# Performance work log

Measured on AMD Instinct MI355X. Metric: run time of the kernel, lower is better.

## Reference

```python
import jax, jax.numpy as jnp
import numpy as np

N = 50000      # nodes
E = 800000     # edges
C = 32         # channels (in = hidden = out, hardcoded in module)
KS = 4         # spline kernel size per dim
K = KS ** 3    # total spline kernel weights (dim=3)
H = 8          # NodeFormer heads
DH = C // H    # head dim = 4
M = 32         # random features for softmax kernel
EPS = 1e-5
SLOPE = 0.01   # LeakyReLU default
TAU = 1.0      # forward default


def seg_sum(vals, segs, num):
    return jax.ops.segment_sum(vals, segs, num_segments=num)


def leaky(x):
    return jnp.where(x >= 0, x, SLOPE * x)


def batch_norm(x, gamma, beta):
    # BatchNorm1d in training mode over the node dim (biased variance)
    mu = x.mean(0)
    var = x.var(0)
    return (x - mu) * jax.lax.rsqrt(var + EPS) * gamma + beta


def spline_conv(x, edge_index, pseudo, w_kernel, w_root, bias):
    # Degree-1 open B-spline conv (torch_spline_conv semantics), mean aggregation.
    src, dst = edge_index[0], edge_index[1]
    x_src = x[src]                                  # [E, C] gather
    p = pseudo * (KS - 1)                           # [E, 3], pseudo in [0,1]
    f = jnp.clip(jnp.floor(p), 0, KS - 2).astype(jnp.int32)
    frac = p - f                                    # [E, 3]
    buf = jnp.zeros((N * K, C), x.dtype)            # [N*K, C] per-kernel scatter buffer
    for bits in range(8):                           # 2^dim nonzero basis products
        idx = jnp.zeros(E, jnp.int32)
        basis = jnp.ones(E, x.dtype)
        for d in range(3):
            bit = (bits >> d) & 1
            idx = idx + (f[:, d] + bit) * (KS ** d)
            basis = basis * (frac[:, d] if bit else (1.0 - frac[:, d]))
        buf = buf + seg_sum(basis[:, None] * x_src, dst.astype(jnp.int32) * K + idx, N * K)
    buf = buf.reshape(N, K, C)
    deg = jnp.clip(seg_sum(jnp.ones(E, x.dtype), dst, N), 1.0)
    out = jnp.einsum('nkc,kcd->nd', buf, w_kernel) / deg[:, None]
    return out + x @ w_root + bias


def softmax_kernel(x, wp):
    # Positive random-feature map approximating the softmax kernel. x: [N,H,DH]
    xn = x / (DH ** 0.25)
    proj = jnp.einsum('nhd,hdm->nhm', xn, wp)
    sq = 0.5 * jnp.sum(xn * xn, -1, keepdims=True)
    return jnp.exp(proj - sq) / np.float32(np.sqrt(M))


def nodeformer_conv(x, edge_index, wqkv, wp, b_rel, wo, bo, gumbel, tau):
    # Kernelized Gumbel-softmax linear attention over all nodes + edge relational bias.
    q = jnp.einsum('nc,chd->nhd', x, wqkv[0])
    k = jnp.einsum('nc,chd->nhd', x, wqkv[1])
    v = jnp.einsum('nc,chd->nhd', x, wqkv[2])
    phi_q = softmax_kernel(q, wp)                              # [N,H,M]
    phi_k = softmax_kernel(k, wp) * jnp.exp(gumbel / tau)      # gumbel: [N,H,1]
    kv = jnp.einsum('nhm,nhd->hmd', phi_k, v)                  # [H,M,DH] summary
    num = jnp.einsum('nhm,hmd->nhd', phi_q, kv)
    den = jnp.einsum('nhm,hm->nh', phi_q, phi_k.sum(0)) + 1e-6
    attn = num / den[..., None]                                # [N,H,DH]
    # relational bias along observed edges (deg-normalized message passing)
    src, dst = edge_index[0], edge_index[1]
    deg = jnp.clip(seg_sum(jnp.ones(E, x.dtype), dst, N), 1.0)
    norm_e = jax.lax.rsqrt(deg[src] * deg[dst])
    rel = seg_sum(v[src] * norm_e[:, None, None], dst, N)      # [N,H,DH]
    out = attn + jax.nn.sigmoid(b_rel)[None, :, None] * rel
    return out.reshape(N, H * DH) @ wo + bo


def setup_inputs() -> dict:
    key = jax.random.key(0)
    ks = jax.random.split(key, 24)
    s_k = np.float32(1.0 / np.sqrt(C))
    inp = {
        'patch_embs': jax.random.normal(ks[0], (N, C), jnp.float32),
        'edge_index': jax.random.randint(ks[1], (2, E), 0, N),
        'edge_attr': jax.random.uniform(ks[2], (E, 3), jnp.float32),
        # SplineConv 1 & 2 params
        'w_sp1': jax.random.normal(ks[3], (K, C, C), jnp.float32) * s_k,
        'root1': jax.random.normal(ks[4], (C, C), jnp.float32) * s_k,
        'bias1': jnp.zeros((C,), jnp.float32),
        'w_sp2': jax.random.normal(ks[5], (K, C, C), jnp.float32) * s_k,
        'root2': jax.random.normal(ks[6], (C, C), jnp.float32) * s_k,
        'bias2': jnp.zeros((C,), jnp.float32),
        # 4 BatchNorm layers, packed
        'bn_gamma': jnp.ones((4, C), jnp.float32),
        'bn_beta': jnp.zeros((4, C), jnp.float32),
        # NodeFormer layer 1
        'nf1_wqkv': jax.random.normal(ks[7], (3, C, H, DH), jnp.float32) * s_k,
        'nf1_wp': jax.random.normal(ks[8], (H, DH, M), jnp.float32),
        'nf1_brel': jnp.zeros((H,), jnp.float32),
        'nf1_wo': jax.random.normal(ks[9], (H * DH, C), jnp.float32) * s_k,
        'nf1_bo': jnp.zeros((C,), jnp.float32),
        'gumbel1': -jnp.log(-jnp.log(jax.random.uniform(ks[10], (N, H, 1), jnp.float32) + 1e-9) + 1e-9),
        # NodeFormer layer 2
        'nf2_wqkv': jax.random.normal(ks[11], (3, C, H, DH), jnp.float32) * s_k,
        'nf2_wp': jax.random.normal(ks[12], (H, DH, M), jnp.float32),
        'nf2_brel': jnp.zeros((H,), jnp.float32),
        'nf2_wo': jax.random.normal(ks[13], (H * DH, C), jnp.float32) * s_k,
        'nf2_bo': jnp.zeros((C,), jnp.float32),
        'gumbel2': -jnp.log(-jnp.log(jax.random.uniform(ks[14], (N, H, 1), jnp.float32) + 1e-9) + 1e-9),
    }
    return inp


def reference(patch_embs, edge_index, edge_attr,
              w_sp1, root1, bias1, w_sp2, root2, bias2,
              bn_gamma, bn_beta,
              nf1_wqkv, nf1_wp, nf1_brel, nf1_wo, nf1_bo, gumbel1,
              nf2_wqkv, nf2_wp, nf2_brel, nf2_wo, nf2_bo, gumbel2):
    x = batch_norm(leaky(spline_conv(patch_embs, edge_index, edge_attr, w_sp1, root1, bias1)), bn_gamma[0], bn_beta[0])
    x = batch_norm(leaky(spline_conv(x, edge_index, edge_attr, w_sp2, root2, bias2)), bn_gamma[1], bn_beta[1])
    x = batch_norm(leaky(nodeformer_conv(x, edge_index, nf1_wqkv, nf1_wp, nf1_brel, nf1_wo, nf1_bo, gumbel1, TAU)), bn_gamma[2], bn_beta[2])
    x = batch_norm(nodeformer_conv(x, edge_index, nf2_wqkv, nf2_wp, nf2_brel, nf2_wo, nf2_bo, gumbel2, TAU), bn_gamma[3], bn_beta[3])
    return x
```

## Files before the change

### kernel.cpp

```cpp
#include <hip/hip_runtime.h>
#include <hip/hip_bf16.h>
#include <hip/hip_fp16.h>

#define NN 50000
#define NE 800000

__device__ __forceinline__ void gAdd(float* p, float v) {
    unsafeAtomicAdd(p, v);
}
__device__ __forceinline__ unsigned short f2bf(float f) {
    unsigned u = __float_as_uint(f);
    u += 0x7FFF + ((u >> 16) & 1);
    return (unsigned short)(u >> 16);
}

__global__ void k_hist(const int* __restrict__ ei, int* __restrict__ cnt) {
    int e = blockIdx.x * 256 + threadIdx.x;
    atomicAdd(&cnt[ei[NE + e]], 1);
}

__global__ void __launch_bounds__(1024) k_scan(const int* __restrict__ cnt,
                                               int* __restrict__ rowptr,
                                               int* __restrict__ fill,
                                               float* __restrict__ degf) {
    __shared__ int wsum[16];
    int tid = threadIdx.x;
    int wave = tid >> 6, lane = tid & 63;
    int carry = 0;
    for (int base = 0; base < NN; base += 8192) {
        int i0 = base + tid * 8;
        int v[8], pre[8], s = 0;
#pragma unroll
        for (int j = 0; j < 8; j++) {
            int i = i0 + j;
            v[j] = (i < NN) ? cnt[i] : 0;
            pre[j] = s; s += v[j];
        }
        int sc = s;
#pragma unroll
        for (int d = 1; d < 64; d <<= 1) {
            int t = __shfl_up(sc, d);
            if (lane >= d) sc += t;
        }
        if (lane == 63) wsum[wave] = sc;
        __syncthreads();
        int wpre = 0, total = 0;
#pragma unroll
        for (int w = 0; w < 16; w++) {
            int x = wsum[w];
            if (w < wave) wpre += x;
            total += x;
        }
        int excl = carry + wpre + (sc - s);
#pragma unroll
        for (int j = 0; j < 8; j++) {
            int i = i0 + j;
            if (i < NN) {
                int st = excl + pre[j];
                rowptr[i] = st;
                fill[i]   = st;
                degf[i]   = (float)(v[j] > 0 ? v[j] : 1);
                if (i == NN - 1) rowptr[NN] = st + v[j];
            }
        }
        carry += total;
        __syncthreads();
    }
}

__global__ void k_scatter(const int* __restrict__ ei, const float* __restrict__ attr,
                          const float* __restrict__ degf,
                          int* __restrict__ fill, int* __restrict__ sedgeP,
                          float2* __restrict__ re2) {
    int e = blockIdx.x * 256 + threadIdx.x;
    int src = ei[e], dst = ei[NE + e];
    int pos = atomicAdd(&fill[dst], 1);
    float p0 = attr[e * 3 + 0] * 3.f, p1 = attr[e * 3 + 1] * 3.f, p2 = attr[e * 3 + 2] * 3.f;
    float f0 = fmaxf(fminf(floorf(p0), 2.f), 0.f);
    float f1 = fmaxf(fminf(floorf(p1), 2.f), 0.f);
    float f2 = fmaxf(fminf(floorf(p2), 2.f), 0.f);
    float r0 = p0 - f0, r1 = p1 - f1, r2 = p2 - f2;
    int idxb = (int)f0 + 4 * (int)f1 + 16 * (int)f2;
    unsigned hw[8];
#pragma unroll
    for (int bits = 0; bits < 8; bits++) {
        int b0 = bits & 1, b1 = (bits >> 1) & 1, b2 = (bits >> 2) & 1;
        float bas = (b0 ? r0 : 1.f - r0) * (b1 ? r1 : 1.f - r1) * (b2 ? r2 : 1.f - r2);
        hw[bits] = (unsigned)__half_as_ushort(__float2half(bas));
    }
    int b = pos * 8;
    sedgeP[b + 0] = src;
    sedgeP[b + 1] = idxb;
    sedgeP[b + 2] = (int)(hw[0] | (hw[1] << 16));
    sedgeP[b + 3] = (int)(hw[2] | (hw[3] << 16));
    sedgeP[b + 4] = (int)(hw[4] | (hw[5] << 16));
    sedgeP[b + 5] = (int)(hw[6] | (hw[7] << 16));
    re2[pos] = make_float2(__int_as_float(src), rsqrtf(degf[src] * degf[dst]));
}

__global__ void k_cvt(const float* __restrict__ xin, unsigned short* __restrict__ xh) {
    int i = blockIdx.x * 256 + threadIdx.x;
    xh[i] = f2bf(xin[i]);
}

__global__ void __launch_bounds__(256) k_spline(
        const float* __restrict__ xin, const unsigned short* __restrict__ xh,
        const int* __restrict__ rowptr,
        const int* __restrict__ sedgeP, const float* __restrict__ degf,
        const float* __restrict__ wsp, const float* __restrict__ root,
        const float* __restrict__ bias, float* __restrict__ out,
        float* __restrict__ stats) {
    __shared__ __align__(16) float buf[8192];
    __shared__ __align__(16) float xt[4][32];
    __shared__ __align__(16) float scr[1024];
    __shared__ float scr2[2][64];
    int tid = threadIdx.x;
    int wave = tid >> 6, lane = tid & 63;
    for (int i = tid; i < 8192; i += 256) buf[i] = 0.f;
    int nb = blockIdx.x * 4;
    if (tid < 128) {
        int t = tid >> 5, c = tid & 31;
        xt[t][c] = xin[(nb + t) * 32 + c];
    }
    __syncthreads();
    {
        int n = nb + wave;
        int rs = rowptr[n], re = rowptr[n + 1];
        int ch = lane & 31, hi = lane >> 5;
        int tof = wave << 5;
        for (int ce = rs; ce < re; ce += 64) {
            int cnt = re - ce; if (cnt > 64) cnt = 64;
            int2 hdr = make_int2(0, 0);
            if (lane < cnt) hdr = *(const int2*)&sedgeP[(ce + lane) * 8];
            int mysrc = hdr.x, myidxb = hdr.y;
            for (int j0 = 0; j0 < cnt; j0 += 8) {
                float xsv[8]; int ib2[8]; uint2 wp[8];
#pragma unroll
                for (int jj = 0; jj < 8; jj++) {
                    int j = j0 + jj;
                    int s  = __shfl(mysrc, j);
                    int ib = __shfl(myidxb, j);
                    int ok = (j < cnt);
                    int sc = ok ? s : 0;
                    int je = ce + (ok ? j : 0);
                    unsigned short u = xh[sc * 32 + ch];
                    xsv[jj] = __uint_as_float(((unsigned)u) << 16);
                    ib2[jj] = ib + (hi << 4);
                    wp[jj]  = *(const uint2*)&sedgeP[je * 8 + 2 + hi * 2];
                }
#pragma unroll
                for (int jj = 0; jj < 8; jj++) {
                    int j = j0 + jj;
                    if (j < cnt) {
                        uint2 w = wp[jj];
                        float xs = xsv[jj];
                        float b0 = __half2float(__ushort_as_half((unsigned short)(w.x & 0xFFFF)));
                        float b1 = __half2float(__ushort_as_half((unsigned short)(w.x >> 16)));
                        float b2 = __half2float(__ushort_as_half((unsigned short)(w.y & 0xFFFF)));
                        float b3 = __half2float(__ushort_as_half((unsigned short)(w.y >> 16)));
                        int i0 = ib2[jj], i1 = i0 + 1, i2 = i0 + 4, i3 = i0 + 5;
                        int a0 = (i0 << 7) + tof + (ch ^ ((i0 & 7) << 2));
                        int a1 = (i1 << 7) + tof + (ch ^ ((i1 & 7) << 2));
                        int a2 = (i2 << 7) + tof + (ch ^ ((i2 & 7) << 2));
                        int a3 = (i3 << 7) + tof + (ch ^ ((i3 & 7) << 2));
                        float v0 = buf[a0], v1 = buf[a1], v2 = buf[a2], v3 = buf[a3];
                        buf[a0] = v0 + b0 * xs;
                        buf[a1] = v1 + b1 * xs;
                        buf[a2] = v2 + b2 * xs;
                        buf[a3] = v3 + b3 * xs;
                    }
                }
            }
        }
    }
    __syncthreads();
    int kk = lane >> 3, d8 = lane & 7;
    float4 acc[2][4];
#pragma unroll
    for (int hf = 0; hf < 2; hf++)
#pragma unroll
        for (int t = 0; t < 4; t++) acc[hf][t] = make_float4(0.f, 0.f, 0.f, 0.f);
#pragma unroll
    for (int hf = 0; hf < 2; hf++) {
        int k = hf * 32 + wave * 8 + kk;
        const float* wk = wsp + k * 1024;
#pragma unroll
        for (int c4 = 0; c4 < 8; c4++) {
            float4 wv0 = *(const float4*)(wk + (c4 * 4 + 0) * 32 + d8 * 4);
            float4 wv1 = *(const float4*)(wk + (c4 * 4 + 1) * 32 + d8 * 4);
            float4 wv2 = *(const float4*)(wk + (c4 * 4 + 2) * 32 + d8 * 4);
            float4 wv3 = *(const float4*)(wk + (c4 * 4 + 3) * 32 + d8 * 4);
            int cp = (c4 ^ kk) << 2;
            const float* bp = &buf[(k * 4) << 5];
#pragma unroll
            for (int t = 0; t < 4; t++) {
                float4 bv = *(const float4*)(bp + (t << 5) + cp);
                acc[hf][t].x += bv.x * wv0.x + bv.y * wv1.x + bv.z * wv2.x + bv.w * wv3.x;
                acc[hf][t].y += bv.x * wv0.y + bv.y * wv1.y + bv.z * wv2.y + bv.w * wv3.y;
                acc[hf][t].z += bv.x * wv0.z + bv.y * wv1.z + bv.z * wv2.z + bv.w * wv3.z;
                acc[hf][t].w += bv.x * wv0.w + bv.y * wv1.w + bv.z * wv2.w + bv.w * wv3.w;
            }
        }
    }
#pragma unroll
    for (int hf = 0; hf < 2; hf++)
#pragma unroll
    for (int t = 0; t < 4; t++) {
        float sx = acc[hf][t].x, sy = acc[hf][t].y, sz = acc[hf][t].z, sw = acc[hf][t].w;
        sx += __shfl_xor(sx, 8);  sy += __shfl_xor(sy, 8);  sz += __shfl_xor(sz, 8);  sw += __shfl_xor(sw, 8);
        sx += __shfl_xor(sx, 16); sy += __shfl_xor(sy, 16); sz += __shfl_xor(sz, 16); sw += __shfl_xor(sw, 16);
        sx += __shfl_xor(sx, 32); sy += __shfl_xor(sy, 32); sz += __shfl_xor(sz, 32); sw += __shfl_xor(sw, 32);
        acc[hf][t] = make_float4(sx, sy, sz, sw);
    }
    if (kk == 0) {
#pragma unroll
        for (int hf = 0; hf < 2; hf++)
#pragma unroll
        for (int t = 0; t < 4; t++)
            *(float4*)&scr[(wave * 2 + hf) * 128 + d8 * 16 + t * 4] = acc[hf][t];
    }
    __syncthreads();
    if (tid < 128) {
        int t = tid >> 5, d = tid & 31;
        int n = nb + t;
        float v = 0.f;
#pragma unroll
        for (int wh = 0; wh < 8; wh++)
            v += scr[wh * 128 + (d >> 2) * 16 + t * 4 + (d & 3)];
        v /= degf[n];
        float rt = 0.f;
#pragma unroll
        for (int c = 0; c < 32; c++) rt += xt[t][c] * root[c * 32 + d];
        v += rt + bias[d];
        v = v >= 0.f ? v : 0.01f * v;
        out[n * 32 + d] = v;
        float s = v, s2 = v * v;
        s += __shfl_xor(s, 32); s2 += __shfl_xor(s2, 32);
        if ((tid & 63) < 32) {
            scr2[tid >> 6][d] = s;
            scr2[tid >> 6][32 + d] = s2;
        }
    }
    __syncthreads();
    if (tid < 64) gAdd(&stats[(blockIdx.x & 63) * 64 + tid], scr2[0][tid] + scr2[1][tid]);
}

__global__ void k_bn(const float* __restrict__ tin, const float* __restrict__ stats,
                     const float* __restrict__ gamma, const float* __restrict__ beta,
                     float* __restrict__ xout) {
    __shared__ float fl[64];
    int tid = threadIdx.x;
    if (tid < 64) {
        float s = 0.f;
#pragma unroll 8
        for (int r = 0; r < 64; r++) s += stats[r * 64 + tid];
        fl[tid] = s;
    }
    __syncthreads();
    int i = blockIdx.x * 256 + tid;
    int c = i & 31;
    float mu = fl[c] * (1.f / NN);
    float var = fl[32 + c] * (1.f / NN) - mu * mu;
    float g = gamma[c] * rsqrtf(var + 1e-5f);
    xout[i] = (tin[i] - mu) * g + beta[c];
}
__global__ void k_bn_cvt(const float* __restrict__ tin, const float* __restrict__ stats,
                         const float* __restrict__ gamma, const float* __restrict__ beta,
                         float* __restrict__ xout, unsigned short* __restrict__ xh) {
    __shared__ float fl[64];
    int tid = threadIdx.x;
    if (tid < 64) {
        float s = 0.f;
#pragma unroll 8
        for (int r = 0; r < 64; r++) s += stats[r * 64 + tid];
        fl[tid] = s;
    }
    __syncthreads();
    int i = blockIdx.x * 256 + tid;
    int c = i & 31;
    float mu = fl[c] * (1.f / NN);
    float var = fl[32 + c] * (1.f / NN) - mu * mu;
    float g = gamma[c] * rsqrtf(var + 1e-5f);
    float v = (tin[i] - mu) * g + beta[c];
    xout[i] = v;
    xh[i] = f2bf(v);
}

__global__ void __launch_bounds__(256) k_nf1(
        const float* __restrict__ x, const float* __restrict__ wqkv,
        const float* __restrict__ wp, const float* __restrict__ gumbel,
        unsigned short* __restrict__ vh, float* __restrict__ kvg) {
    __shared__ float xl[32 * 33];
    __shared__ __align__(16) float kq[32][8][4];
    __shared__ __align__(16) float vv[32][8][4];
    __shared__ float sqv[32][8];
    __shared__ float gsv[32][8];
    int tid = threadIdx.x;
    int base = blockIdx.x * 32;
#pragma unroll
    for (int r = 0; r < 4; r++) {
        int i = r * 256 + tid;
        int gi = base * 32 + i;
        float v = (gi < NN * 32) ? x[gi] : 0.f;
        xl[(i >> 5) * 33 + (i & 31)] = v;
    }
    __syncthreads();
    int nl = tid >> 3, h = tid & 7;
    int n = base + nl;
    int act = (n < NN) ? 1 : 0;
    const float* xp = &xl[nl * 33];
    float kr0 = 0, kr1 = 0, kr2 = 0, kr3 = 0, vr0 = 0, vr1 = 0, vr2 = 0, vr3 = 0;
#pragma unroll
    for (int c = 0; c < 32; c++) {
        float xc = xp[c];
        const float4 wk4 = *(const float4*)(wqkv + 1024 + c * 32 + h * 4);
        const float4 wv4 = *(const float4*)(wqkv + 2048 + c * 32 + h * 4);
        kr0 += xc * wk4.x; kr1 += xc * wk4.y; kr2 += xc * wk4.z; kr3 += xc * wk4.w;
        vr0 += xc * wv4.x; vr1 += xc * wv4.y; vr2 += xc * wv4.z; vr3 += xc * wv4.w;
    }
    if (act) {
        unsigned lo = (unsigned)f2bf(vr0) | ((unsigned)f2bf(vr1) << 16);
        unsigned hi_ = (unsigned)f2bf(vr2) | ((unsigned)f2bf(vr3) << 16);
        *(uint2*)&vh[n * 32 + h * 4] = make_uint2(lo, hi_);
    }
    const float inv_rt2 = 0.70710678118f;
    const float invSqM = 0.17677669529f;
    float x0 = kr0 * inv_rt2, x1 = kr1 * inv_rt2, x2 = kr2 * inv_rt2, x3 = kr3 * inv_rt2;
    float sq = 0.5f * (x0 * x0 + x1 * x1 + x2 * x2 + x3 * x3);
    float gs = act ? (__expf(gumbel[(act ? n : 0) * 8 + h]) * invSqM) : 0.f;
    *(float4*)&kq[nl][h][0] = make_float4(x0, x1, x2, x3);
    *(float4*)&vv[nl][h][0] = make_float4(vr0, vr1, vr2, vr3);
    sqv[nl][h] = sq;
    gsv[nl][h] = gs;
    __syncthreads();
    int h2 = tid >> 5, m = tid & 31;
    const float* wph = wp + h2 * 128;
    float w0 = wph[m], w1 = wph[32 + m], w2 = wph[64 + m], w3 = wph[96 + m];
    float ks = 0.f, a0 = 0.f, a1 = 0.f, a2 = 0.f, a3 = 0.f;
#pragma unroll 4
    for (int nn2 = 0; nn2 < 32; nn2++) {
        float4 k4 = *(const float4*)&kq[nn2][h2][0];
        float4 v4 = *(const float4*)&vv[nn2][h2][0];
        float pr = k4.x * w0 + k4.y * w1 + k4.z * w2 + k4.w * w3;
        float phk = __expf(pr - sqv[nn2][h2]) * gsv[nn2][h2];
        ks += phk;
        a0 += phk * v4.x; a1 += phk * v4.y; a2 += phk * v4.z; a3 += phk * v4.w;
    }
    float* kvr = kvg + (blockIdx.x & 7) * 1280;
    gAdd(&kvr[1024 + h2 * 32 + m], ks);
    gAdd(&kvr[0 * 256 + h2 * 32 + m], a0);
    gAdd(&kvr[1 * 256 + h2 * 32 + m], a1);
    gAdd(&kvr[2 * 256 + h2 * 32 + m], a2);
    gAdd(&kvr[3 * 256 + h2 * 32 + m], a3);
}

__global__ void __launch_bounds__(256) k_nf2(
        const float* __restrict__ x, const float* __restrict__ wqkv,
        const float* __restrict__ wp, const float* __restrict__ brel,
        const float* __restrict__ wo, const float* __restrict__ bo,
        const float* __restrict__ kvg, const int* __restrict__ rowptr,
        const float2* __restrict__ re2, const unsigned short* __restrict__ vh,
        int do_leaky, float* __restrict__ out, float* __restrict__ stats) {
    __shared__ float xl[32 * 33];
    __shared__ float ylds[32 * 33];
    __shared__ float kvs[1280];
    __shared__ float scr2[4][64];
    int tid = threadIdx.x;
    int base = blockIdx.x * 32;
#pragma unroll
    for (int r = 0; r < 4; r++) {
        int i = r * 256 + tid;
        int gi = base * 32 + i;
        float v = (gi < NN * 32) ? x[gi] : 0.f;
        xl[(i >> 5) * 33 + (i & 31)] = v;
    }
    for (int i = tid; i < 1280; i += 256) {
        float s = 0.f;
#pragma unroll
        for (int r = 0; r < 8; r++) s += kvg[r * 1280 + i];
        kvs[i] = s;
    }
    __syncthreads();
    int nl = tid >> 3, h = tid & 7;
    int n = base + nl;
    int act = (n < NN) ? 1 : 0;
    int nc = act ? n : (NN - 1);
    const float* xp = &xl[nl * 33];
    float q0 = 0, q1 = 0, q2 = 0, q3 = 0;
#pragma unroll
    for (int c = 0; c < 32; c++) {
        float xc = xp[c];
        const float4 wq4 = *(const float4*)(wqkv + c * 32 + h * 4);
        q0 += xc * wq4.x; q1 += xc * wq4.y; q2 += xc * wq4.z; q3 += xc * wq4.w;
    }
    const float inv_rt2 = 0.70710678118f;
    const float invSqM = 0.17677669529f;
    float x0 = q0 * inv_rt2, x1 = q1 * inv_rt2, x2 = q2 * inv_rt2, x3 = q3 * inv_rt2;
    float sq = 0.5f * (x0 * x0 + x1 * x1 + x2 * x2 + x3 * x3);
    const float* wph = wp + h * 128;
    float den = 0.f, n0 = 0.f, n1 = 0.f, n2 = 0.f, n3 = 0.f;
    for (int mm = 0; mm < 32; mm++) {
        int m = (mm + 4 * h) & 31;
        float pr = x0 * wph[m] + x1 * wph[32 + m] + x2 * wph[64 + m] + x3 * wph[96 + m];
        float phq = __expf(pr - sq) * invSqM;
        den += phq * kvs[1024 + h * 32 + m];
        n0 += phq * kvs[0 * 256 + h * 32 + m];
        n1 += phq * kvs[1 * 256 + h * 32 + m];
        n2 += phq * kvs[2 * 256 + h * 32 + m];
        n3 += phq * kvs[3 * 256 + h * 32 + m];
    }
    float inv = 1.f / (den + 1e-6f);
    float y0 = n0 * inv, y1 = n1 * inv, y2 = n2 * inv, y3 = n3 * inv;
    float r0 = 0, r1 = 0, r2 = 0, r3 = 0;
    int rs = rowptr[nc];
    int re = act ? rowptr[nc + 1] : rs;
    int lb = (tid & 63) & 56;
    for (int e0 = rs; e0 < re; e0 += 8) {
        int cnt = re - e0; if (cnt > 8) cnt = 8;
        float2 med = make_float2(__int_as_float(0), 0.f);
        if (h < cnt) med = re2[e0 + h];
        int msrc = __float_as_int(med.x);
        uint2 xs4[8];
        float nrj[8];
#pragma unroll
        for (int jj = 0; jj < 8; jj++) {
            int s   = __shfl(msrc, lb + jj);
            float nr = __shfl(med.y, lb + jj);
            nrj[jj] = (jj < cnt) ? nr : 0.f;
            int sc  = (jj < cnt) ? s : 0;
            xs4[jj] = *(const uint2*)&vh[sc * 32 + h * 4];
        }
#pragma unroll
        for (int jj = 0; jj < 8; jj++) {
            uint2 u = xs4[jj];
            r0 += nrj[jj] * __uint_as_float(u.x << 16);
            r1 += nrj[jj] * __uint_as_float(u.x & 0xFFFF0000u);
            r2 += nrj[jj] * __uint_as_float(u.y << 16);
            r3 += nrj[jj] * __uint_as_float(u.y & 0xFFFF0000u);
        }
    }
    float sg = 1.f / (1.f + __expf(-brel[h]));
    y0 += sg * r0; y1 += sg * r1; y2 += sg * r2; y3 += sg * r3;
    ylds[nl * 33 + h * 4 + 0] = y0;
    ylds[nl * 33 + h * 4 + 1] = y1;
    ylds[nl * 33 + h * 4 + 2] = y2;
    ylds[nl * 33 + h * 4 + 3] = y3;
    __syncthreads();
    const float* yp = &ylds[nl * 33];
    const float4 b4 = *(const float4*)(bo + h * 4);
    float z0 = b4.x, z1 = b4.y, z2 = b4.z, z3 = b4.w;
#pragma unroll
    for (int j = 0; j < 32; j++) {
        float yv = yp[j];
        const float4 w4 = *(const float4*)(wo + j * 32 + h * 4);
        z0 += yv * w4.x; z1 += yv * w4.y; z2 += yv * w4.z; z3 += yv * w4.w;
    }
    if (do_leaky) {
        z0 = z0 >= 0.f ? z0 : 0.01f * z0;
        z1 = z1 >= 0.f ? z1 : 0.01f * z1;
        z2 = z2 >= 0.f ? z2 : 0.01f * z2;
        z3 = z3 >= 0.f ? z3 : 0.01f * z3;
    }
    if (act) *(float4*)&out[n * 32 + h * 4] = make_float4(z0, z1, z2, z3);
    int wv = tid >> 6;
    float sv[4] = {act ? z0 : 0.f, act ? z1 : 0.f, act ? z2 : 0.f, act ? z3 : 0.f};
#pragma unroll
    for (int j = 0; j < 4; j++) {
        float s = sv[j], s2 = sv[j] * sv[j];
        s += __shfl_xor(s, 8);  s2 += __shfl_xor(s2, 8);
        s += __shfl_xor(s, 16); s2 += __shfl_xor(s2, 16);
        s += __shfl_xor(s, 32); s2 += __shfl_xor(s2, 32);
        if (((tid & 63) >> 3) == 0) {
            scr2[wv][h * 4 + j] = s;
            scr2[wv][32 + h * 4 + j] = s2;
        }
    }
    __syncthreads();
    if (tid < 64)
        gAdd(&stats[(blockIdx.x & 63) * 64 + tid],
             scr2[0][tid] + scr2[1][tid] + scr2[2][tid] + scr2[3][tid]);
}

extern "C" void kernel_launch(void* const* d_in, const int* in_sizes, int n_in,
                              void* d_out, int out_size, void* d_ws, size_t ws_size,
                              hipStream_t stream) {
    (void)in_sizes; (void)n_in; (void)out_size; (void)ws_size;
    const float* x_in  = (const float*)d_in[0];
    const int*   ei    = (const int*)d_in[1];
    const float* attr  = (const float*)d_in[2];
    const float* wsp1  = (const float*)d_in[3];
    const float* root1 = (const float*)d_in[4];
    const float* bias1 = (const float*)d_in[5];
    const float* wsp2  = (const float*)d_in[6];
    const float* root2 = (const float*)d_in[7];
    const float* bias2 = (const float*)d_in[8];
    const float* gam   = (const float*)d_in[9];
    const float* bet   = (const float*)d_in[10];
    const float* w1qkv = (const float*)d_in[11];
    const float* w1p   = (const float*)d_in[12];
    const float* b1rel = (const float*)d_in[13];
    const float* w1o   = (const float*)d_in[14];
    const float* b1o   = (const float*)d_in[15];
    const float* gum1  = (const float*)d_in[16];
    const float* w2qkv = (const float*)d_in[17];
    const float* w2p   = (const float*)d_in[18];
    const float* b2rel = (const float*)d_in[19];
    const float* w2o   = (const float*)d_in[20];
    const float* b2o   = (const float*)d_in[21];
    const float* gum2  = (const float*)d_in[22];
    float* outp = (float*)d_out;

    char* wsb = (char*)d_ws;
    size_t off = 0;
    auto carve = [&](size_t bytes) -> char* {
        char* p = wsb + off;
        off += (bytes + 255) & ~(size_t)255;
        return p;
    };
    int*    cnt    = (int*)carve((size_t)NN * 4);
    float*  kvg1   = (float*)carve(8 * 1280 * 4);
    float*  kvg2   = (float*)carve(8 * 1280 * 4);
    float*  stats  = (float*)carve(4 * 64 * 64 * 4);
    size_t zero_bytes = off;
    int*    rowptr = (int*)carve((size_t)(NN + 1) * 4);
    int*    fill   = (int*)carve((size_t)NN * 4);
    float*  degf   = (float*)carve((size_t)NN * 4);
    int*    sedgeP = (int*)carve((size_t)NE * 32);
    float2* re2    = (float2*)carve((size_t)NE * 8);
    unsigned short* xh0 = (unsigned short*)carve((size_t)NN * 32 * 2);
    unsigned short* xah = (unsigned short*)carve((size_t)NN * 32 * 2);
    unsigned short* vh  = (unsigned short*)carve((size_t)NN * 32 * 2);
    float*  xa     = (float*)carve((size_t)NN * 32 * 4);
    float*  xb     = (float*)carve((size_t)NN * 32 * 4);
    float*  tb     = (float*)carve((size_t)NN * 32 * 4);

    hipMemsetAsync(d_ws, 0, zero_bytes, stream);
    k_hist<<<NE / 256, 256, 0, stream>>>(ei, cnt);
    k_scan<<<1, 1024, 0, stream>>>(cnt, rowptr, fill, degf);
    k_scatter<<<NE / 256, 256, 0, stream>>>(ei, attr, degf, fill, sedgeP, re2);
    k_cvt<<<NN * 32 / 256, 256, 0, stream>>>(x_in, xh0);

    k_spline<<<NN / 4, 256, 0, stream>>>(x_in, xh0, rowptr, sedgeP, degf, wsp1, root1, bias1, tb, stats);
    k_bn_cvt<<<NN * 32 / 256, 256, 0, stream>>>(tb, stats, gam, bet, xa, xah);
    k_spline<<<NN / 4, 256, 0, stream>>>(xa, xah, rowptr, sedgeP, degf, wsp2, root2, bias2, tb, stats + 4096);
    k_bn<<<NN * 32 / 256, 256, 0, stream>>>(tb, stats + 4096, gam + 32, bet + 32, xb);

    int nfgrid = (NN + 31) / 32;
    k_nf1<<<nfgrid, 256, 0, stream>>>(xb, w1qkv, w1p, gum1, vh, kvg1);
    k_nf2<<<nfgrid, 256, 0, stream>>>(xb, w1qkv, w1p, b1rel, w1o, b1o, kvg1, rowptr, re2,
                                      vh, 1, tb, stats + 8192);
    k_bn<<<NN * 32 / 256, 256, 0, stream>>>(tb, stats + 8192, gam + 64, bet + 64, xa);
    k_nf1<<<nfgrid, 256, 0, stream>>>(xa, w2qkv, w2p, gum2, vh, kvg2);
    k_nf2<<<nfgrid, 256, 0, stream>>>(xa, w2qkv, w2p, b2rel, w2o, b2o, kvg2, rowptr, re2,
                                      vh, 0, tb, stats + 12288);
    k_bn<<<NN * 32 / 256, 256, 0, stream>>>(tb, stats + 12288, gam + 96, bet + 96, outp);
}
```

Baseline: 1.250 ms.

## Shrink spline block to two nodes and split LDS accumulator into two buffers

The spline conv kernel now processes two nodes per 128-thread block instead of four per 256 threads. The per-node kernel accumulation buffer is split into two interleaved halves, alternating by edge parity, to break read-modify-write dependency chains on LDS. The halves are summed before the dense weight contraction, which is re-tiled so each wave covers four k-groups. LDS per block stays about 32KB for half the nodes, so wsp weights are reloaded twice as often per node and occupancy may be limited.

```diff
diff --git a/kernel.cpp b/kernel.cpp
--- a/kernel.cpp
+++ b/kernel.cpp
@@ -103,22 +103,23 @@
     xh[i] = f2bf(xin[i]);
 }
 
-__global__ void __launch_bounds__(256) k_spline(
+__global__ void __launch_bounds__(128) k_spline(
         const float* __restrict__ xin, const unsigned short* __restrict__ xh,
         const int* __restrict__ rowptr,
         const int* __restrict__ sedgeP, const float* __restrict__ degf,
         const float* __restrict__ wsp, const float* __restrict__ root,
         const float* __restrict__ bias, float* __restrict__ out,
         float* __restrict__ stats) {
-    __shared__ __align__(16) float buf[8192];
-    __shared__ __align__(16) float xt[4][32];
-    __shared__ __align__(16) float scr[1024];
-    __shared__ float scr2[2][64];
+    __shared__ __align__(16) float bufA[4096];
+    __shared__ __align__(16) float bufB[4096];
+    __shared__ __align__(16) float xt[2][32];
+    __shared__ __align__(16) float scr[512];
+    __shared__ float scr2[64];
     int tid = threadIdx.x;
     int wave = tid >> 6, lane = tid & 63;
-    for (int i = tid; i < 8192; i += 256) buf[i] = 0.f;
-    int nb = blockIdx.x * 4;
-    if (tid < 128) {
+    for (int i = tid; i < 4096; i += 128) { bufA[i] = 0.f; bufB[i] = 0.f; }
+    int nb = blockIdx.x * 2;
+    if (tid < 64) {
         int t = tid >> 5, c = tid & 31;
         xt[t][c] = xin[(nb + t) * 32 + c];
     }
@@ -152,6 +153,7 @@
                 for (int jj = 0; jj < 8; jj++) {
                     int j = j0 + jj;
                     if (j < cnt) {
+                        float* bb = (jj & 1) ? bufB : bufA;
                         uint2 w = wp[jj];
                         float xs = xsv[jj];
                         float b0 = __half2float(__ushort_as_half((unsigned short)(w.x & 0xFFFF)));
@@ -159,30 +161,32 @@
                         float b2 = __half2float(__ushort_as_half((unsigned short)(w.y & 0xFFFF)));
                         float b3 = __half2float(__ushort_as_half((unsigned short)(w.y >> 16)));
                         int i0 = ib2[jj], i1 = i0 + 1, i2 = i0 + 4, i3 = i0 + 5;
-                        int a0 = (i0 << 7) + tof + (ch ^ ((i0 & 7) << 2));
-                        int a1 = (i1 << 7) + tof + (ch ^ ((i1 & 7) << 2));
-                        int a2 = (i2 << 7) + tof + (ch ^ ((i2 & 7) << 2));
-                        int a3 = (i3 << 7) + tof + (ch ^ ((i3 & 7) << 2));
-                        float v0 = buf[a0], v1 = buf[a1], v2 = buf[a2], v3 = buf[a3];
-                        buf[a0] = v0 + b0 * xs;
-                        buf[a1] = v1 + b1 * xs;
-                        buf[a2] = v2 + b2 * xs;
-                        buf[a3] = v3 + b3 * xs;
+                        int a0 = (i0 << 6) + tof + (ch ^ ((i0 & 7) << 2));
+                        int a1 = (i1 << 6) + tof + (ch ^ ((i1 & 7) << 2));
+                        int a2 = (i2 << 6) + tof + (ch ^ ((i2 & 7) << 2));
+                        int a3 = (i3 << 6) + tof + (ch ^ ((i3 & 7) << 2));
+                        float v0 = bb[a0], v1 = bb[a1], v2 = bb[a2], v3 = bb[a3];
+                        bb[a0] = v0 + b0 * xs;
+                        bb[a1] = v1 + b1 * xs;
+                        bb[a2] = v2 + b2 * xs;
+                        bb[a3] = v3 + b3 * xs;
                     }
                 }
             }
         }
     }
     __syncthreads();
+    for (int i = tid; i < 4096; i += 128) bufA[i] += bufB[i];
+    __syncthreads();
     int kk = lane >> 3, d8 = lane & 7;
-    float4 acc[2][4];
-#pragma unroll
-    for (int hf = 0; hf < 2; hf++)
-#pragma unroll
-        for (int t = 0; t < 4; t++) acc[hf][t] = make_float4(0.f, 0.f, 0.f, 0.f);
-#pragma unroll
-    for (int hf = 0; hf < 2; hf++) {
-        int k = hf * 32 + wave * 8 + kk;
+    float4 acc[4][2];
+#pragma unroll
+    for (int hf = 0; hf < 4; hf++)
+#pragma unroll
+        for (int t = 0; t < 2; t++) acc[hf][t] = make_float4(0.f, 0.f, 0.f, 0.f);
+#pragma unroll
+    for (int hf = 0; hf < 4; hf++) {
+        int k = hf * 16 + wave * 8 + kk;
         const float* wk = wsp + k * 1024;
 #pragma unroll
         for (int c4 = 0; c4 < 8; c4++) {
@@ -191,9 +195,9 @@
             float4 wv2 = *(const float4*)(wk + (c4 * 4 + 2) * 32 + d8 * 4);
             float4 wv3 = *(const float4*)(wk + (c4 * 4 + 3) * 32 + d8 * 4);
             int cp = (c4 ^ kk) << 2;
-            const float* bp = &buf[(k * 4) << 5];
-#pragma unroll
-            for (int t = 0; t < 4; t++) {
+            const float* bp = &bufA[(k * 2) << 5];
+#pragma unroll
+            for (int t = 0; t < 2; t++) {
                 float4 bv = *(const float4*)(bp + (t << 5) + cp);
                 acc[hf][t].x += bv.x * wv0.x + bv.y * wv1.x + bv.z * wv2.x + bv.w * wv3.x;
                 acc[hf][t].y += bv.x * wv0.y + bv.y * wv1.y + bv.z * wv2.y + bv.w * wv3.y;
@@ -203,9 +207,9 @@
         }
     }
 #pragma unroll
-    for (int hf = 0; hf < 2; hf++)
-#pragma unroll
-    for (int t = 0; t < 4; t++) {
+    for (int hf = 0; hf < 4; hf++)
+#pragma unroll
+    for (int t = 0; t < 2; t++) {
         float sx = acc[hf][t].x, sy = acc[hf][t].y, sz = acc[hf][t].z, sw = acc[hf][t].w;
         sx += __shfl_xor(sx, 8);  sy += __shfl_xor(sy, 8);  sz += __shfl_xor(sz, 8);  sw += __shfl_xor(sw, 8);
         sx += __shfl_xor(sx, 16); sy += __shfl_xor(sy, 16); sz += __shfl_xor(sz, 16); sw += __shfl_xor(sw, 16);
@@ -214,19 +218,19 @@
     }
     if (kk == 0) {
 #pragma unroll
-        for (int hf = 0; hf < 2; hf++)
-#pragma unroll
-        for (int t = 0; t < 4; t++)
-            *(float4*)&scr[(wave * 2 + hf) * 128 + d8 * 16 + t * 4] = acc[hf][t];
-    }
-    __syncthreads();
-    if (tid < 128) {
+        for (int hf = 0; hf < 4; hf++)
+#pragma unroll
+        for (int t = 0; t < 2; t++)
+            *(float4*)&scr[(wave * 4 + hf) * 64 + d8 * 8 + t * 4] = acc[hf][t];
+    }
+    __syncthreads();
+    if (tid < 64) {
         int t = tid >> 5, d = tid & 31;
         int n = nb + t;
         float v = 0.f;
 #pragma unroll
-        for (int wh = 0; wh < 8; wh++)
-            v += scr[wh * 128 + (d >> 2) * 16 + t * 4 + (d & 3)];
+        for (int g = 0; g < 8; g++)
+            v += scr[g * 64 + (d >> 2) * 8 + t * 4 + (d & 3)];
         v /= degf[n];
         float rt = 0.f;
 #pragma unroll
@@ -236,13 +240,10 @@
         out[n * 32 + d] = v;
         float s = v, s2 = v * v;
         s += __shfl_xor(s, 32); s2 += __shfl_xor(s2, 32);
-        if ((tid & 63) < 32) {
-            scr2[tid >> 6][d] = s;
-            scr2[tid >> 6][32 + d] = s2;
-        }
-    }
-    __syncthreads();
-    if (tid < 64) gAdd(&stats[(blockIdx.x & 63) * 64 + tid], scr2[0][tid] + scr2[1][tid]);
+        if (tid < 32) { scr2[d] = s; scr2[32 + d] = s2; }
+    }
+    __syncthreads();
+    if (tid < 64) gAdd(&stats[(blockIdx.x & 63) * 64 + tid], scr2[tid]);
 }
 
 __global__ void k_bn(const float* __restrict__ tin, const float* __restrict__ stats,
@@ -540,9 +541,9 @@
     k_scatter<<<NE / 256, 256, 0, stream>>>(ei, attr, degf, fill, sedgeP, re2);
     k_cvt<<<NN * 32 / 256, 256, 0, stream>>>(x_in, xh0);
 
-    k_spline<<<NN / 4, 256, 0, stream>>>(x_in, xh0, rowptr, sedgeP, degf, wsp1, root1, bias1, tb, stats);
+    k_spline<<<NN / 2, 128, 0, stream>>>(x_in, xh0, rowptr, sedgeP, degf, wsp1, root1, bias1, tb, stats);
     k_bn_cvt<<<NN * 32 / 256, 256, 0, stream>>>(tb, stats, gam, bet, xa, xah);
-    k_spline<<<NN / 4, 256, 0, stream>>>(xa, xah, rowptr, sedgeP, degf, wsp2, root2, bias2, tb, stats + 4096);
+    k_spline<<<NN / 2, 128, 0, stream>>>(xa, xah, rowptr, sedgeP, degf, wsp2, root2, bias2, tb, stats + 4096);
     k_bn<<<NN * 32 / 256, 256, 0, stream>>>(tb, stats + 4096, gam + 32, bet + 32, xb);
 
     int nfgrid = (NN + 31) / 32;
```

New measurement: 1.675 ms. 1.34x slower.
